# Kernel tuning notes

Hardware: AMD Instinct MI355X
Metric: run time of the kernel (lower is better)

The kernel has to match this reference:

```python
import jax, jax.numpy as jnp
import numpy as np

N_NODES = 100000
N_EDGES = 3200000


def gcn_conv(x, edge_index, W, b, n):
    # PyG GCNConv: h = x @ W; add self-loops; symmetric deg normalization; scatter-add; + bias
    src = edge_index[0]
    dst = edge_index[1]
    loop = jnp.arange(n, dtype=src.dtype)
    src = jnp.concatenate([src, loop])
    dst = jnp.concatenate([dst, loop])
    ones = jnp.ones(src.shape[0], dtype=x.dtype)
    deg = jax.ops.segment_sum(ones, dst, num_segments=n)  # in-degree with self-loops
    dinv = jnp.where(deg > 0, jax.lax.rsqrt(deg), 0.0)
    norm = dinv[src] * dinv[dst]  # [E+N]
    h = x @ W  # [N, out]
    msg = h[src] * norm[:, None]
    out = jax.ops.segment_sum(msg, dst, num_segments=n)
    return out + b


def setup_inputs() -> dict:
    key = jax.random.key(0)
    ks = jax.random.split(key, 8)
    x = jax.random.normal(ks[0], (N_NODES, 1024), dtype=jnp.float32)
    edge_index = jax.random.randint(ks[1], (2, N_EDGES), 0, N_NODES, dtype=jnp.int32)
    def glorot(k, fan_in, fan_out):
        s = jnp.sqrt(6.0 / (fan_in + fan_out))
        return jax.random.uniform(k, (fan_in, fan_out), jnp.float32, -s, s)
    W1 = glorot(ks[2], 1024, 128)
    W2 = glorot(ks[3], 128, 128)
    W3 = glorot(ks[4], 128, 9)
    b1 = jnp.zeros((128,), jnp.float32)
    b2 = jnp.zeros((128,), jnp.float32)
    b3 = jnp.zeros((9,), jnp.float32)
    return {"x": x, "edge_index": edge_index, "W1": W1, "b1": b1, "W2": W2, "b2": b2, "W3": W3, "b3": b3}


def reference(x, edge_index, W1, b1, W2, b2, W3, b3):
    n = x.shape[0]
    h = jax.nn.relu(gcn_conv(x, edge_index, W1, b1, n))
    h = jax.nn.relu(gcn_conv(h, edge_index, W2, b2, n))
    h = gcn_conv(h, edge_index, W3, b3, n)
    return jax.nn.log_softmax(h, axis=1)
```

## Files before the change

### kernel.cpp

```cpp
#include <hip/hip_runtime.h>
#include <hip/hip_bf16.h>

typedef __attribute__((ext_vector_type(8))) short bf16x8;
typedef __attribute__((ext_vector_type(4))) float f32x4;

#define BSH 8
#define BNODES 256

__device__ __forceinline__ unsigned short f2bf(float f) {
    union { float f; unsigned int u; } x; x.f = f;
    unsigned int u = x.u;
    unsigned int r = (u + 0x7fffu + ((u >> 16) & 1u)) >> 16;
    return (unsigned short)r;
}
__device__ __forceinline__ float bf_lo(unsigned int v) { return __uint_as_float(v << 16); }
__device__ __forceinline__ float bf_hi(unsigned int v) { return __uint_as_float(v & 0xffff0000u); }

__device__ __forceinline__ void gll16(const void* g, void* l) {
    __builtin_amdgcn_global_load_lds(
        (const __attribute__((address_space(1))) unsigned int*)g,
        (__attribute__((address_space(3))) unsigned int*)l, 16, 0, 0);
}


__global__ void k_zero(int* p, int n) {
    int i = blockIdx.x * 256 + threadIdx.x;
    if (i < n) p[i] = 0;
}

__global__ __launch_bounds__(256) void kA_hist(const int* __restrict__ dst, int* bhist,
                                               int E, int nbkt) {
    __shared__ int h[512];
    for (int i = threadIdx.x; i < 512; i += 256) h[i] = 0;
    __syncthreads();
    int stride = gridDim.x * 256;
    int n4 = E >> 2;
    for (int i = blockIdx.x * 256 + threadIdx.x; i < n4; i += stride) {
        int4 d = ((const int4*)dst)[i];
        atomicAdd(&h[d.x >> BSH], 1);
        atomicAdd(&h[d.y >> BSH], 1);
        atomicAdd(&h[d.z >> BSH], 1);
        atomicAdd(&h[d.w >> BSH], 1);
    }
    for (int i = (n4 << 2) + blockIdx.x * 256 + threadIdx.x; i < E; i += stride)
        atomicAdd(&h[dst[i] >> BSH], 1);
    __syncthreads();
    for (int i = threadIdx.x; i < nbkt; i += 256)
        if (h[i]) atomicAdd(&bhist[i], h[i]);
}

__global__ void kA_scan(const int* bhist, int* bbase, int* bcur, int nbkt) {
    __shared__ int s[512];
    int t = threadIdx.x;
    int v = (t < nbkt) ? bhist[t] : 0;
    s[t] = v;
    __syncthreads();
    for (int o = 1; o < 512; o <<= 1) {
        int x = (t >= o) ? s[t - o] : 0;
        __syncthreads();
        s[t] += x;
        __syncthreads();
    }
    if (t < nbkt) { bbase[t] = s[t] - v; bcur[t] = s[t] - v; }
    if (t == nbkt - 1) bbase[nbkt] = s[t];
}

#define TPE 16
__global__ __launch_bounds__(256) void kA_scatter(const int* __restrict__ src,
                                                  const int* __restrict__ dst,
                                                  int* bcur, unsigned int* pairs,
                                                  int E, int nbkt) {
    __shared__ int hist[512];
    __shared__ int base[512];
    const int tid = threadIdx.x;
    const int t0 = blockIdx.x * (256 * TPE);
    for (int i = tid; i < 512; i += 256) hist[i] = 0;
    __syncthreads();

    int es[TPE], ed[TPE], rk[TPE];
    bool valid[TPE];
    if (t0 + 256 * TPE <= E) {
        const int4* s4 = (const int4*)(src + t0 + tid * TPE);
        const int4* d4 = (const int4*)(dst + t0 + tid * TPE);
#pragma unroll
        for (int j = 0; j < TPE / 4; j++) {
            int4 a = s4[j], b = d4[j];
            es[4 * j + 0] = a.x; es[4 * j + 1] = a.y; es[4 * j + 2] = a.z; es[4 * j + 3] = a.w;
            ed[4 * j + 0] = b.x; ed[4 * j + 1] = b.y; ed[4 * j + 2] = b.z; ed[4 * j + 3] = b.w;
            valid[4 * j + 0] = valid[4 * j + 1] = valid[4 * j + 2] = valid[4 * j + 3] = true;
        }
    } else {
#pragma unroll
        for (int j = 0; j < TPE; j++) {
            int e = t0 + tid * TPE + j;
            valid[j] = (e < E);
            es[j] = valid[j] ? src[e] : 0;
            ed[j] = valid[j] ? dst[e] : 0;
        }
    }
#pragma unroll
    for (int j = 0; j < TPE; j++)
        if (valid[j]) rk[j] = atomicAdd(&hist[ed[j] >> BSH], 1);
    __syncthreads();
    for (int i = tid; i < nbkt; i += 256) {
        int c = hist[i];
        base[i] = c ? atomicAdd(&bcur[i], c) : 0;
    }
    __syncthreads();
#pragma unroll
    for (int j = 0; j < TPE; j++) {
        if (valid[j]) {
            int b = ed[j] >> BSH;
            unsigned int p = ((unsigned int)(ed[j] & (BNODES - 1)) << 24) | (unsigned int)es[j];
            pairs[base[b] + rk[j]] = p;
        }
    }
}

__global__ __launch_bounds__(512) void kB_group(const unsigned int* __restrict__ pairs,
                                                const int* __restrict__ bbase,
                                                int* csr, int* offs, int* cnt, float* dinv,
                                                int N, int nbkt) {
    int b = blockIdx.x;
    int p0 = bbase[b], p1 = bbase[b + 1];
    int node0 = b << BSH;
    int nn = min(BNODES, N - node0);
    __shared__ int lcnt[BNODES];
    __shared__ int ss[BNODES];
    __shared__ int lcur[BNODES];
    int t = threadIdx.x;
    if (t < BNODES) lcnt[t] = 0;
    __syncthreads();
    for (int i = p0 + t; i < p1; i += 512)
        atomicAdd(&lcnt[pairs[i] >> 24], 1);
    __syncthreads();
    int v = (t < BNODES) ? lcnt[t] : 0;
    if (t < BNODES) ss[t] = v;
    __syncthreads();
    for (int o = 1; o < BNODES; o <<= 1) {
        int x = (t >= o && t < BNODES) ? ss[t - o] : 0;
        __syncthreads();
        if (t < BNODES) ss[t] += x;
        __syncthreads();
    }
    if (t < nn) {
        int o = p0 + ss[t] - v;
        offs[node0 + t] = o;
        cnt[node0 + t] = v;
        dinv[node0 + t] = rsqrtf((float)(v + 1));
        lcur[t] = o;
    }
    __syncthreads();
    for (int i = p0 + t; i < p1; i += 512) {
        unsigned int p = pairs[i];
        int pos = atomicAdd(&lcur[p >> 24], 1);
        csr[pos] = (int)(p & 0xFFFFFFu);
    }
}

__global__ void k_wt(const float* W, unsigned short* Wt, int K, int C) {
    int i = blockIdx.x * 256 + threadIdx.x;
    if (i < K * C) {
        int k = i / C, c = i % C;
        Wt[(size_t)c * K + k] = f2bf(W[i]);
    }
}


template <int K, bool IN_F32>
__global__ __launch_bounds__(256) void k_gemm(const void* Xv, const unsigned short* Wt,
                                              const float* dinv, unsigned short* G, int M) {
    constexpr int ABYTES = IN_F32 ? 128 * 32 * 4 : 128 * 32 * 2;
    constexpr int BBYTES = 128 * 32 * 2;
    constexpr int NT = K / 32;
    __shared__ char smem[2 * ABYTES + 2 * BBYTES];

    const int tid = threadIdx.x;
    const int m0 = blockIdx.x * 128;
    const int w = tid >> 6, l = tid & 63, r = l & 15, kg = l >> 4;
    const int wb0 = tid & ~63;

    auto stage = [&](int buf, int k0) {
        if (IN_F32) {
            const float* X = (const float*)Xv;
            char* ab = smem + buf * ABYTES;
#pragma unroll
            for (int i = 0; i < 4; i++) {
                int wb = i * 256 + wb0;
                int c = wb + l;
                int row = c >> 3, slot = c & 7;
                int srow = m0 + row; if (srow >= M) srow = M - 1;
                gll16(X + (size_t)srow * K + k0 + slot * 4, ab + (size_t)wb * 16);
            }
        } else {
            const unsigned short* X = (const unsigned short*)Xv;
            char* ab = smem + buf * ABYTES;
#pragma unroll
            for (int i = 0; i < 2; i++) {
                int wb = i * 256 + wb0;
                int c = wb + l;
                int row = c >> 2, slot = c & 3;
                int srow = m0 + row; if (srow >= M) srow = M - 1;
                gll16(X + (size_t)srow * K + k0 + slot * 8, ab + (size_t)wb * 16);
            }
        }
        {
            char* bb = smem + 2 * ABYTES + buf * BBYTES;
#pragma unroll
            for (int i = 0; i < 2; i++) {
                int wb = i * 256 + wb0;
                int c = wb + l;
                int row = c >> 2, slot = c & 3;
                gll16(Wt + (size_t)row * K + k0 + slot * 8, bb + (size_t)wb * 16);
            }
        }
    };

    f32x4 acc[2][8];
#pragma unroll
    for (int mt = 0; mt < 2; mt++)
#pragma unroll
        for (int ct = 0; ct < 8; ct++) acc[mt][ct] = (f32x4){0.f, 0.f, 0.f, 0.f};

    stage(0, 0);
    __syncthreads();

    int cur = 0;
    for (int t = 0; t < NT; t++) {
        if (t + 1 < NT) stage(cur ^ 1, (t + 1) * 32);

        bf16x8 af[2], bfr[8];
        if (IN_F32) {
            const float* ab = (const float*)(smem + cur * ABYTES);
#pragma unroll
            for (int mt = 0; mt < 2; mt++) {
                int row = w * 32 + mt * 16 + r;
                float4 f0 = *(const float4*)(ab + row * 32 + kg * 8);
                float4 f1 = *(const float4*)(ab + row * 32 + kg * 8 + 4);
                union { bf16x8 v; unsigned short u[8]; } a;
                a.u[0] = f2bf(f0.x); a.u[1] = f2bf(f0.y); a.u[2] = f2bf(f0.z); a.u[3] = f2bf(f0.w);
                a.u[4] = f2bf(f1.x); a.u[5] = f2bf(f1.y); a.u[6] = f2bf(f1.z); a.u[7] = f2bf(f1.w);
                af[mt] = a.v;
            }
        } else {
            const unsigned short* ab = (const unsigned short*)(smem + cur * ABYTES);
#pragma unroll
            for (int mt = 0; mt < 2; mt++) {
                int row = w * 32 + mt * 16 + r;
                af[mt] = *(const bf16x8*)(ab + row * 32 + kg * 8);
            }
        }
        {
            const unsigned short* bb = (const unsigned short*)(smem + 2 * ABYTES + cur * BBYTES);
#pragma unroll
            for (int ct = 0; ct < 8; ct++)
                bfr[ct] = *(const bf16x8*)(bb + (ct * 16 + r) * 32 + kg * 8);
        }
#pragma unroll
        for (int mt = 0; mt < 2; mt++)
#pragma unroll
            for (int ct = 0; ct < 8; ct++)
                acc[mt][ct] = __builtin_amdgcn_mfma_f32_16x16x32_bf16(af[mt], bfr[ct], acc[mt][ct], 0, 0, 0);

        __syncthreads();
        cur ^= 1;
    }

#pragma unroll
    for (int mt = 0; mt < 2; mt++) {
        int rbase = m0 + w * 32 + mt * 16 + kg * 4;
        float dv[4];
#pragma unroll
        for (int q = 0; q < 4; q++) dv[q] = (rbase + q < M) ? dinv[rbase + q] : 0.f;
#pragma unroll
        for (int ct = 0; ct < 8; ct++) {
#pragma unroll
            for (int q = 0; q < 4; q++) {
                int gr = rbase + q;
                if (gr < M) G[(size_t)gr * 128 + ct * 16 + r] = f2bf(acc[mt][ct][q] * dv[q]);
            }
        }
    }
}


__global__ __launch_bounds__(256) void k_gemm3(const unsigned short* X3, const float* W3,
                                               const float* dinv, unsigned short* G3, int M) {
    __shared__ unsigned short sx[128 * 136];
    __shared__ float sw[128 * 9];
    int tid = threadIdx.x;
    int m0 = blockIdx.x * 128;
#pragma unroll
    for (int p = 0; p < 8; p++) {
        int idx = p * 256 + tid;
        int row = idx >> 4, c8 = idx & 15;
        uint4 v = make_uint4(0u, 0u, 0u, 0u);
        if (m0 + row < M) v = *(const uint4*)(X3 + (size_t)(m0 + row) * 128 + c8 * 8);
        *(uint4*)&sx[row * 136 + c8 * 8] = v;
    }
    for (int i = tid; i < 128 * 9; i += 256) sw[i] = W3[i];
    __syncthreads();

    int r = tid >> 1, h = tid & 1;
    float acc[9];
#pragma unroll
    for (int c = 0; c < 9; c++) acc[c] = 0.f;
    for (int kk = 0; kk < 64; kk++) {
        int k = h * 64 + kk;
        float xv = __uint_as_float(((unsigned int)sx[r * 136 + k]) << 16);
#pragma unroll
        for (int c = 0; c < 9; c++) acc[c] += xv * sw[k * 9 + c];
    }
#pragma unroll
    for (int c = 0; c < 9; c++) acc[c] += __shfl_xor(acc[c], 1);
    int gr = m0 + r;
    if (h == 0 && gr < M) {
        float dv = dinv[gr];
#pragma unroll
        for (int c = 0; c < 9; c++) G3[(size_t)gr * 16 + c] = f2bf(acc[c] * dv);
#pragma unroll
        for (int c = 9; c < 16; c++) G3[(size_t)gr * 16 + c] = 0;
    }
}


#define A128_CAP 1024

__global__ __launch_bounds__(256) void k_agg128(const unsigned int* __restrict__ gv,
                                                const int* __restrict__ csr,
                                                const int* __restrict__ offs,
                                                const int* __restrict__ cnt,
                                                const float* __restrict__ dinv,
                                                const float* __restrict__ bias,
                                                unsigned int* xout, int N, int do_relu) {
    __shared__ int sidx[A128_CAP];
    const int tid = threadIdx.x;
    const int n0 = blockIdx.x * 4;
    const int nlast = min(n0 + 3, N - 1);
    const int base = offs[n0];
    const int tot = offs[nlast] + cnt[nlast] - base;
    const bool lds_ok = (tot <= A128_CAP);
    if (lds_ok)
        for (int i = tid; i < tot; i += 256) sidx[i] = csr[base + i];
    __syncthreads();

    const int node = n0 + (tid >> 6);
    if (node >= N) return;
    const int l = tid & 63;
    const int ne = cnt[node];
    const int st = offs[node] - base;

    unsigned int u = gv[node * 64 + l];
    float a0 = bf_lo(u), a1 = bf_hi(u);
    int e = 0;
    if (lds_ok) {
        for (; e + 8 <= ne; e += 8) {
            int s0 = sidx[st + e], s1 = sidx[st + e + 1];
            int s2 = sidx[st + e + 2], s3 = sidx[st + e + 3];
            int s4 = sidx[st + e + 4], s5 = sidx[st + e + 5];
            int s6 = sidx[st + e + 6], s7 = sidx[st + e + 7];
            unsigned int v0 = gv[s0 * 64 + l], v1 = gv[s1 * 64 + l];
            unsigned int v2 = gv[s2 * 64 + l], v3 = gv[s3 * 64 + l];
            unsigned int v4 = gv[s4 * 64 + l], v5 = gv[s5 * 64 + l];
            unsigned int v6 = gv[s6 * 64 + l], v7 = gv[s7 * 64 + l];
            a0 += bf_lo(v0); a1 += bf_hi(v0);
            a0 += bf_lo(v1); a1 += bf_hi(v1);
            a0 += bf_lo(v2); a1 += bf_hi(v2);
            a0 += bf_lo(v3); a1 += bf_hi(v3);
            a0 += bf_lo(v4); a1 += bf_hi(v4);
            a0 += bf_lo(v5); a1 += bf_hi(v5);
            a0 += bf_lo(v6); a1 += bf_hi(v6);
            a0 += bf_lo(v7); a1 += bf_hi(v7);
        }
        for (; e < ne; e++) {
            unsigned int v = gv[sidx[st + e] * 64 + l];
            a0 += bf_lo(v); a1 += bf_hi(v);
        }
    } else {
        const int gst = offs[node];
        for (; e < ne; e++) {
            unsigned int v = gv[csr[gst + e] * 64 + l];
            a0 += bf_lo(v); a1 += bf_hi(v);
        }
    }
    float dv = dinv[node];
    float o0 = fmaf(dv, a0, bias[2 * l]);
    float o1 = fmaf(dv, a1, bias[2 * l + 1]);
    if (do_relu) { o0 = fmaxf(o0, 0.f); o1 = fmaxf(o1, 0.f); }
    xout[node * 64 + l] = (unsigned int)f2bf(o0) | ((unsigned int)f2bf(o1) << 16);
}


#define A9_CAP 3072

__global__ __launch_bounds__(256) void k_agg9(const unsigned int* __restrict__ g3v,
                                              const int* __restrict__ csr,
                                              const int* __restrict__ offs,
                                              const int* __restrict__ cnt,
                                              const float* __restrict__ dinv,
                                              const float* __restrict__ b3,
                                              float* out, int N) {
    __shared__ int sidx[A9_CAP];
    const int tid = threadIdx.x;
    const int n0 = blockIdx.x * 32;
    const int nlast = min(n0 + 31, N - 1);
    const int base = offs[n0];
    const int tot = offs[nlast] + cnt[nlast] - base;
    const bool lds_ok = (tot <= A9_CAP);
    if (lds_ok)
        for (int i = tid; i < tot; i += 256) sidx[i] = csr[base + i];
    __syncthreads();

    const int node = n0 + (tid >> 3);
    if (node >= N) return;
    const int jl = tid & 7;
    const int ne = cnt[node];

    unsigned int u = g3v[node * 8 + jl];
    float a0 = bf_lo(u), a1 = bf_hi(u);
    int e = 0;
    if (lds_ok) {
        const int st = offs[node] - base;
        for (; e + 4 <= ne; e += 4) {
            int s0 = sidx[st + e], s1 = sidx[st + e + 1];
            int s2 = sidx[st + e + 2], s3 = sidx[st + e + 3];
            unsigned int v0 = g3v[s0 * 8 + jl], v1 = g3v[s1 * 8 + jl];
            unsigned int v2 = g3v[s2 * 8 + jl], v3 = g3v[s3 * 8 + jl];
            a0 += bf_lo(v0); a1 += bf_hi(v0);
            a0 += bf_lo(v1); a1 += bf_hi(v1);
            a0 += bf_lo(v2); a1 += bf_hi(v2);
            a0 += bf_lo(v3); a1 += bf_hi(v3);
        }
        for (; e < ne; e++) {
            unsigned int v = g3v[sidx[st + e] * 8 + jl];
            a0 += bf_lo(v); a1 += bf_hi(v);
        }
    } else {
        const int gst = offs[node];
        for (; e < ne; e++) {
            unsigned int v = g3v[csr[gst + e] * 8 + jl];
            a0 += bf_lo(v); a1 += bf_hi(v);
        }
    }
    float dv = dinv[node];
    int c0 = 2 * jl, c1 = 2 * jl + 1;
    float o0 = (c0 < 9) ? fmaf(dv, a0, b3[c0]) : -INFINITY;
    float o1 = (c1 < 9) ? fmaf(dv, a1, b3[c1]) : -INFINITY;
    float m = fmaxf(o0, o1);
    for (int d = 1; d < 8; d <<= 1) m = fmaxf(m, __shfl_xor(m, d));
    float s = 0.f;
    if (c0 < 9) s += expf(o0 - m);
    if (c1 < 9) s += expf(o1 - m);
    for (int d = 1; d < 8; d <<= 1) s += __shfl_xor(s, d);
    float ls = m + logf(s);
    if (c0 < 9) out[(size_t)node * 9 + c0] = o0 - ls;
    if (c1 < 9) out[(size_t)node * 9 + c1] = o1 - ls;
}


extern "C" void kernel_launch(void* const* d_in, const int* in_sizes, int n_in,
                              void* d_out, int out_size, void* d_ws, size_t ws_size,
                              hipStream_t stream) {
    const float* x = (const float*)d_in[0];
    const int* ei = (const int*)d_in[1];
    const float* W1 = (const float*)d_in[2];
    const float* b1 = (const float*)d_in[3];
    const float* W2 = (const float*)d_in[4];
    const float* b2 = (const float*)d_in[5];
    const float* W3 = (const float*)d_in[6];
    const float* b3 = (const float*)d_in[7];
    float* out = (float*)d_out;

    const int N = in_sizes[0] / 1024;
    const int E = in_sizes[1] / 2;
    const int* src = ei;
    const int* dst = ei + E;
    const int nbkt = (N + BNODES - 1) >> BSH;

    char* ws = (char*)d_ws;
    size_t off = 0;
    auto alloc = [&](size_t bytes) -> char* {
        char* p = ws + off;
        off += (bytes + 255) & ~(size_t)255;
        return p;
    };
    int* cnt = (int*)alloc((size_t)N * 4);
    int* offs = (int*)alloc((size_t)N * 4);
    float* dinv = (float*)alloc((size_t)N * 4);
    int* bhist = (int*)alloc(520 * 4);
    int* bbase = (int*)alloc(520 * 4);
    int* bcur = (int*)alloc(520 * 4);
    unsigned int* pairs = (unsigned int*)alloc((size_t)E * 4);
    int* csr = (int*)alloc((size_t)E * 4);
    unsigned short* w1t = (unsigned short*)alloc(128 * 1024 * 2);
    unsigned short* w2t = (unsigned short*)alloc(128 * 128 * 2);
    unsigned short* gbuf = (unsigned short*)alloc((size_t)N * 128 * 2);
    unsigned short* xbuf = (unsigned short*)alloc((size_t)N * 128 * 2);
    unsigned short* g3 = (unsigned short*)alloc((size_t)N * 16 * 2);

    const int MB = (N + 127) / 128;
    const int AB = (N + 3) / 4;
    const int AB9 = (N + 31) / 32;
    const int SB = (E + 256 * TPE - 1) / (256 * TPE);

    k_zero<<<3, 256, 0, stream>>>(bhist, 520);
    kA_hist<<<512, 256, 0, stream>>>(dst, bhist, E, nbkt);
    kA_scan<<<1, 512, 0, stream>>>(bhist, bbase, bcur, nbkt);
    kA_scatter<<<SB, 256, 0, stream>>>(src, dst, bcur, pairs, E, nbkt);
    kB_group<<<nbkt, 512, 0, stream>>>(pairs, bbase, csr, offs, cnt, dinv, N, nbkt);
    k_wt<<<(1024 * 128 + 255) / 256, 256, 0, stream>>>(W1, w1t, 1024, 128);
    k_wt<<<(128 * 128 + 255) / 256, 256, 0, stream>>>(W2, w2t, 128, 128);

    k_gemm<1024, true><<<MB, 256, 0, stream>>>((const void*)x, w1t, dinv, gbuf, N);
    k_agg128<<<AB, 256, 0, stream>>>((const unsigned int*)gbuf, csr, offs, cnt, dinv, b1,
                                     (unsigned int*)xbuf, N, 1);
    k_gemm<128, false><<<MB, 256, 0, stream>>>((const void*)xbuf, w2t, dinv, gbuf, N);
    k_agg128<<<AB, 256, 0, stream>>>((const unsigned int*)gbuf, csr, offs, cnt, dinv, b2,
                                     (unsigned int*)xbuf, N, 1);
    k_gemm3<<<MB, 256, 0, stream>>>(xbuf, W3, dinv, g3, N);
    k_agg9<<<AB9, 256, 0, stream>>>((const unsigned int*)g3, csr, offs, cnt, dinv, b3, out, N);
}
```

Measured before the change: 503.0 us.

## Load GEMM operands directly from global into registers, dropping LDS staging

Replaces the double-buffered global_load_lds staging in the GEMM kernel with per-lane direct global loads of the A rows and the W fragments into registers, removing LDS traffic and block barriers. It also merges the two weight-transpose launches into one kernel. In exchange each wave now reads W fragments from global/L2 on its own, with no reuse through LDS, and the fp32 A loads are strided per lane, which may hurt coalescing and memory-level parallelism.

```diff
diff --git a/kernel.cpp b/kernel.cpp
--- a/kernel.cpp
+++ b/kernel.cpp
@@ -15,12 +15,6 @@
 }
 __device__ __forceinline__ float bf_lo(unsigned int v) { return __uint_as_float(v << 16); }
 __device__ __forceinline__ float bf_hi(unsigned int v) { return __uint_as_float(v & 0xffff0000u); }
-
-__device__ __forceinline__ void gll16(const void* g, void* l) {
-    __builtin_amdgcn_global_load_lds(
-        (const __attribute__((address_space(1))) unsigned int*)g,
-        (__attribute__((address_space(3))) unsigned int*)l, 16, 0, 0);
-}
 
 
 __global__ void k_zero(int* p, int n) {
@@ -158,11 +152,18 @@
     }
 }
 
-__global__ void k_wt(const float* W, unsigned short* Wt, int K, int C) {
+__global__ void k_wt2(const float* __restrict__ W1, unsigned short* w1t,
+                      const float* __restrict__ W2, unsigned short* w2t) {
     int i = blockIdx.x * 256 + threadIdx.x;
-    if (i < K * C) {
-        int k = i / C, c = i % C;
-        Wt[(size_t)c * K + k] = f2bf(W[i]);
+    if (i < 1024 * 128) {
+        int k = i >> 7, c = i & 127;
+        w1t[c * 1024 + k] = f2bf(W1[i]);
+    } else {
+        int j = i - 1024 * 128;
+        if (j < 128 * 128) {
+            int k = j >> 7, c = j & 127;
+            w2t[c * 128 + k] = f2bf(W2[j]);
+        }
     }
 }
 
@@ -170,51 +171,14 @@
 template <int K, bool IN_F32>
 __global__ __launch_bounds__(256) void k_gemm(const void* Xv, const unsigned short* Wt,
                                               const float* dinv, unsigned short* G, int M) {
-    constexpr int ABYTES = IN_F32 ? 128 * 32 * 4 : 128 * 32 * 2;
-    constexpr int BBYTES = 128 * 32 * 2;
-    constexpr int NT = K / 32;
-    __shared__ char smem[2 * ABYTES + 2 * BBYTES];
-
     const int tid = threadIdx.x;
     const int m0 = blockIdx.x * 128;
     const int w = tid >> 6, l = tid & 63, r = l & 15, kg = l >> 4;
-    const int wb0 = tid & ~63;
-
-    auto stage = [&](int buf, int k0) {
-        if (IN_F32) {
-            const float* X = (const float*)Xv;
-            char* ab = smem + buf * ABYTES;
-#pragma unroll
-            for (int i = 0; i < 4; i++) {
-                int wb = i * 256 + wb0;
-                int c = wb + l;
-                int row = c >> 3, slot = c & 7;
-                int srow = m0 + row; if (srow >= M) srow = M - 1;
-                gll16(X + (size_t)srow * K + k0 + slot * 4, ab + (size_t)wb * 16);
-            }
-        } else {
-            const unsigned short* X = (const unsigned short*)Xv;
-            char* ab = smem + buf * ABYTES;
-#pragma unroll
-            for (int i = 0; i < 2; i++) {
-                int wb = i * 256 + wb0;
-                int c = wb + l;
-                int row = c >> 2, slot = c & 3;
-                int srow = m0 + row; if (srow >= M) srow = M - 1;
-                gll16(X + (size_t)srow * K + k0 + slot * 8, ab + (size_t)wb * 16);
-            }
-        }
-        {
-            char* bb = smem + 2 * ABYTES + buf * BBYTES;
-#pragma unroll
-            for (int i = 0; i < 2; i++) {
-                int wb = i * 256 + wb0;
-                int c = wb + l;
-                int row = c >> 2, slot = c & 3;
-                gll16(Wt + (size_t)row * K + k0 + slot * 8, bb + (size_t)wb * 16);
-            }
-        }
-    };
+
+    const int row0 = m0 + w * 32 + r;
+    const int row1 = row0 + 16;
+    const int cr0 = min(row0, M - 1);
+    const int cr1 = min(row1, M - 1);
 
     f32x4 acc[2][8];
 #pragma unroll
@@ -222,48 +186,53 @@
 #pragma unroll
         for (int ct = 0; ct < 8; ct++) acc[mt][ct] = (f32x4){0.f, 0.f, 0.f, 0.f};
 
-    stage(0, 0);
-    __syncthreads();
-
-    int cur = 0;
-    for (int t = 0; t < NT; t++) {
-        if (t + 1 < NT) stage(cur ^ 1, (t + 1) * 32);
-
-        bf16x8 af[2], bfr[8];
-        if (IN_F32) {
-            const float* ab = (const float*)(smem + cur * ABYTES);
-#pragma unroll
-            for (int mt = 0; mt < 2; mt++) {
-                int row = w * 32 + mt * 16 + r;
-                float4 f0 = *(const float4*)(ab + row * 32 + kg * 8);
-                float4 f1 = *(const float4*)(ab + row * 32 + kg * 8 + 4);
-                union { bf16x8 v; unsigned short u[8]; } a;
-                a.u[0] = f2bf(f0.x); a.u[1] = f2bf(f0.y); a.u[2] = f2bf(f0.z); a.u[3] = f2bf(f0.w);
-                a.u[4] = f2bf(f1.x); a.u[5] = f2bf(f1.y); a.u[6] = f2bf(f1.z); a.u[7] = f2bf(f1.w);
-                af[mt] = a.v;
-            }
-        } else {
-            const unsigned short* ab = (const unsigned short*)(smem + cur * ABYTES);
-#pragma unroll
-            for (int mt = 0; mt < 2; mt++) {
-                int row = w * 32 + mt * 16 + r;
-                af[mt] = *(const bf16x8*)(ab + row * 32 + kg * 8);
-            }
-        }
-        {
-            const unsigned short* bb = (const unsigned short*)(smem + 2 * ABYTES + cur * BBYTES);
-#pragma unroll
-            for (int ct = 0; ct < 8; ct++)
-                bfr[ct] = *(const bf16x8*)(bb + (ct * 16 + r) * 32 + kg * 8);
-        }
-#pragma unroll
-        for (int mt = 0; mt < 2; mt++)
-#pragma unroll
-            for (int ct = 0; ct < 8; ct++)
-                acc[mt][ct] = __builtin_amdgcn_mfma_f32_16x16x32_bf16(af[mt], bfr[ct], acc[mt][ct], 0, 0, 0);
-
-        __syncthreads();
-        cur ^= 1;
+    const unsigned short* bp = Wt + (size_t)r * K + kg * 8;
+
+    if (IN_F32) {
+        const float* X = (const float*)Xv;
+        const float* a0 = X + (size_t)cr0 * K + kg * 8;
+        const float* a1 = X + (size_t)cr1 * K + kg * 8;
+#pragma unroll 2
+        for (int k0 = 0; k0 < K; k0 += 32) {
+            float4 f00 = *(const float4*)(a0 + k0);
+            float4 f01 = *(const float4*)(a0 + k0 + 4);
+            float4 f10 = *(const float4*)(a1 + k0);
+            float4 f11 = *(const float4*)(a1 + k0 + 4);
+            bf16x8 bfr[8];
+#pragma unroll
+            for (int ct = 0; ct < 8; ct++)
+                bfr[ct] = *(const bf16x8*)(bp + (size_t)ct * 16 * K + k0);
+            union { bf16x8 v; unsigned short u[8]; } A0, A1;
+            A0.u[0] = f2bf(f00.x); A0.u[1] = f2bf(f00.y); A0.u[2] = f2bf(f00.z); A0.u[3] = f2bf(f00.w);
+            A0.u[4] = f2bf(f01.x); A0.u[5] = f2bf(f01.y); A0.u[6] = f2bf(f01.z); A0.u[7] = f2bf(f01.w);
+            A1.u[0] = f2bf(f10.x); A1.u[1] = f2bf(f10.y); A1.u[2] = f2bf(f10.z); A1.u[3] = f2bf(f10.w);
+            A1.u[4] = f2bf(f11.x); A1.u[5] = f2bf(f11.y); A1.u[6] = f2bf(f11.z); A1.u[7] = f2bf(f11.w);
+#pragma unroll
+            for (int ct = 0; ct < 8; ct++)
+                acc[0][ct] = __builtin_amdgcn_mfma_f32_16x16x32_bf16(A0.v, bfr[ct], acc[0][ct], 0, 0, 0);
+#pragma unroll
+            for (int ct = 0; ct < 8; ct++)
+                acc[1][ct] = __builtin_amdgcn_mfma_f32_16x16x32_bf16(A1.v, bfr[ct], acc[1][ct], 0, 0, 0);
+        }
+    } else {
+        const unsigned short* X = (const unsigned short*)Xv;
+        const unsigned short* a0 = X + (size_t)cr0 * K + kg * 8;
+        const unsigned short* a1 = X + (size_t)cr1 * K + kg * 8;
+#pragma unroll 2
+        for (int k0 = 0; k0 < K; k0 += 32) {
+            bf16x8 af0 = *(const bf16x8*)(a0 + k0);
+            bf16x8 af1 = *(const bf16x8*)(a1 + k0);
+            bf16x8 bfr[8];
+#pragma unroll
+            for (int ct = 0; ct < 8; ct++)
+                bfr[ct] = *(const bf16x8*)(bp + (size_t)ct * 16 * K + k0);
+#pragma unroll
+            for (int ct = 0; ct < 8; ct++)
+                acc[0][ct] = __builtin_amdgcn_mfma_f32_16x16x32_bf16(af0, bfr[ct], acc[0][ct], 0, 0, 0);
+#pragma unroll
+            for (int ct = 0; ct < 8; ct++)
+                acc[1][ct] = __builtin_amdgcn_mfma_f32_16x16x32_bf16(af1, bfr[ct], acc[1][ct], 0, 0, 0);
+        }
     }
 
 #pragma unroll
@@ -502,14 +471,14 @@
     const int AB = (N + 3) / 4;
     const int AB9 = (N + 31) / 32;
     const int SB = (E + 256 * TPE - 1) / (256 * TPE);
+    const int WB = (1024 * 128 + 128 * 128 + 255) / 256;
 
     k_zero<<<3, 256, 0, stream>>>(bhist, 520);
     kA_hist<<<512, 256, 0, stream>>>(dst, bhist, E, nbkt);
     kA_scan<<<1, 512, 0, stream>>>(bhist, bbase, bcur, nbkt);
     kA_scatter<<<SB, 256, 0, stream>>>(src, dst, bcur, pairs, E, nbkt);
     kB_group<<<nbkt, 512, 0, stream>>>(pairs, bbase, csr, offs, cnt, dinv, N, nbkt);
-    k_wt<<<(1024 * 128 + 255) / 256, 256, 0, stream>>>(W1, w1t, 1024, 128);
-    k_wt<<<(128 * 128 + 255) / 256, 256, 0, stream>>>(W2, w2t, 128, 128);
+    k_wt2<<<WB, 256, 0, stream>>>(W1, w1t, W2, w2t);
 
     k_gemm<1024, true><<<MB, 256, 0, stream>>>((const void*)x, w1t, dinv, gbuf, N);
     k_agg128<<<AB, 256, 0, stream>>>((const unsigned int*)gbuf, csr, offs, cnt, dinv, b1,
```

New measurement: 591.1 us. 17.5% more time.

## Deepen GEMM prefetch to four LDS buffers with vmcnt waits; fuse weight transposes

Applied to the files above, without the earlier changes.

The bf16 MFMA GEMM moves from a double-buffered loop with a full __syncthreads per tile to a four-buffer ring. Three tiles are prefetched ahead with global_load_lds, and each step waits on an explicit s_waitcnt vmcnt count plus a bare s_barrier. The goal is to keep more global loads in flight, mainly in the layer-1 GEMM that streams the large fp32 input. The trade-off is that LDS per block doubles, which can lower occupancy, and correctness now depends on the hand-counted vmcnt values. The two weight-transpose launches are also merged into one kernel to save a launch.

```diff
diff --git a/kernel.cpp b/kernel.cpp
--- a/kernel.cpp
+++ b/kernel.cpp
@@ -20,6 +20,15 @@
     __builtin_amdgcn_global_load_lds(
         (const __attribute__((address_space(1))) unsigned int*)g,
         (__attribute__((address_space(3))) unsigned int*)l, 16, 0, 0);
+}
+
+template <int N> __device__ __forceinline__ void waitvm() {
+    if constexpr (N == 0) asm volatile("s_waitcnt vmcnt(0)" ::: "memory");
+    else if constexpr (N == 4) asm volatile("s_waitcnt vmcnt(4)" ::: "memory");
+    else if constexpr (N == 6) asm volatile("s_waitcnt vmcnt(6)" ::: "memory");
+    else if constexpr (N == 8) asm volatile("s_waitcnt vmcnt(8)" ::: "memory");
+    else if constexpr (N == 12) asm volatile("s_waitcnt vmcnt(12)" ::: "memory");
+    else static_assert(N == 0, "unhandled vmcnt");
 }
 
 
@@ -158,22 +167,34 @@
     }
 }
 
-__global__ void k_wt(const float* W, unsigned short* Wt, int K, int C) {
+__global__ void k_wt2(const float* __restrict__ W1, unsigned short* w1t,
+                      const float* __restrict__ W2, unsigned short* w2t) {
     int i = blockIdx.x * 256 + threadIdx.x;
-    if (i < K * C) {
-        int k = i / C, c = i % C;
-        Wt[(size_t)c * K + k] = f2bf(W[i]);
+    if (i < 1024 * 128) {
+        int k = i >> 7, c = i & 127;
+        w1t[c * 1024 + k] = f2bf(W1[i]);
+    } else {
+        int j = i - 1024 * 128;
+        if (j < 128 * 128) {
+            int k = j >> 7, c = j & 127;
+            w2t[c * 128 + k] = f2bf(W2[j]);
+        }
     }
 }
 
 
 template <int K, bool IN_F32>
-__global__ __launch_bounds__(256) void k_gemm(const void* Xv, const unsigned short* Wt,
-                                              const float* dinv, unsigned short* G, int M) {
+__global__ __launch_bounds__(256) void k_gemm(const void* __restrict__ Xv,
+                                              const unsigned short* __restrict__ Wt,
+                                              const float* __restrict__ dinv,
+                                              unsigned short* __restrict__ G, int M) {
     constexpr int ABYTES = IN_F32 ? 128 * 32 * 4 : 128 * 32 * 2;
     constexpr int BBYTES = 128 * 32 * 2;
     constexpr int NT = K / 32;
-    __shared__ char smem[2 * ABYTES + 2 * BBYTES];
+    constexpr int NBUF = 4;
+    constexpr int L = IN_F32 ? 6 : 4;
+    static_assert(NT >= 3, "pipeline needs >=3 tiles");
+    __shared__ char smem[NBUF * (ABYTES + BBYTES)];
 
     const int tid = threadIdx.x;
     const int m0 = blockIdx.x * 128;
@@ -205,7 +226,7 @@
             }
         }
         {
-            char* bb = smem + 2 * ABYTES + buf * BBYTES;
+            char* bb = smem + NBUF * ABYTES + buf * BBYTES;
 #pragma unroll
             for (int i = 0; i < 2; i++) {
                 int wb = i * 256 + wb0;
@@ -222,16 +243,10 @@
 #pragma unroll
         for (int ct = 0; ct < 8; ct++) acc[mt][ct] = (f32x4){0.f, 0.f, 0.f, 0.f};
 
-    stage(0, 0);
-    __syncthreads();
-
-    int cur = 0;
-    for (int t = 0; t < NT; t++) {
-        if (t + 1 < NT) stage(cur ^ 1, (t + 1) * 32);
-
+    auto compute = [&](int buf) {
         bf16x8 af[2], bfr[8];
         if (IN_F32) {
-            const float* ab = (const float*)(smem + cur * ABYTES);
+            const float* ab = (const float*)(smem + buf * ABYTES);
 #pragma unroll
             for (int mt = 0; mt < 2; mt++) {
                 int row = w * 32 + mt * 16 + r;
@@ -243,7 +258,7 @@
                 af[mt] = a.v;
             }
         } else {
-            const unsigned short* ab = (const unsigned short*)(smem + cur * ABYTES);
+            const unsigned short* ab = (const unsigned short*)(smem + buf * ABYTES);
 #pragma unroll
             for (int mt = 0; mt < 2; mt++) {
                 int row = w * 32 + mt * 16 + r;
@@ -251,7 +266,7 @@
             }
         }
         {
-            const unsigned short* bb = (const unsigned short*)(smem + 2 * ABYTES + cur * BBYTES);
+            const unsigned short* bb = (const unsigned short*)(smem + NBUF * ABYTES + buf * BBYTES);
 #pragma unroll
             for (int ct = 0; ct < 8; ct++)
                 bfr[ct] = *(const bf16x8*)(bb + (ct * 16 + r) * 32 + kg * 8);
@@ -261,10 +276,28 @@
 #pragma unroll
             for (int ct = 0; ct < 8; ct++)
                 acc[mt][ct] = __builtin_amdgcn_mfma_f32_16x16x32_bf16(af[mt], bfr[ct], acc[mt][ct], 0, 0, 0);
-
-        __syncthreads();
-        cur ^= 1;
-    }
+    };
+
+    stage(0, 0);
+    stage(1, 32);
+    stage(2, 64);
+
+    int t = 0;
+    for (; t + 3 < NT; ++t) {
+        waitvm<2 * L>();
+        __builtin_amdgcn_s_barrier();
+        compute(t & 3);
+        stage((t + 3) & 3, (t + 3) * 32);
+    }
+    waitvm<2 * L>();
+    __builtin_amdgcn_s_barrier();
+    compute((NT - 3) & 3);
+    waitvm<L>();
+    __builtin_amdgcn_s_barrier();
+    compute((NT - 2) & 3);
+    waitvm<0>();
+    __builtin_amdgcn_s_barrier();
+    compute((NT - 1) & 3);
 
 #pragma unroll
     for (int mt = 0; mt < 2; mt++) {
@@ -502,14 +535,14 @@
     const int AB = (N + 3) / 4;
     const int AB9 = (N + 31) / 32;
     const int SB = (E + 256 * TPE - 1) / (256 * TPE);
+    const int WB = (1024 * 128 + 128 * 128 + 255) / 256;
 
     k_zero<<<3, 256, 0, stream>>>(bhist, 520);
     kA_hist<<<512, 256, 0, stream>>>(dst, bhist, E, nbkt);
     kA_scan<<<1, 512, 0, stream>>>(bhist, bbase, bcur, nbkt);
     kA_scatter<<<SB, 256, 0, stream>>>(src, dst, bcur, pairs, E, nbkt);
     kB_group<<<nbkt, 512, 0, stream>>>(pairs, bbase, csr, offs, cnt, dinv, N, nbkt);
-    k_wt<<<(1024 * 128 + 255) / 256, 256, 0, stream>>>(W1, w1t, 1024, 128);
-    k_wt<<<(128 * 128 + 255) / 256, 256, 0, stream>>>(W2, w2t, 128, 128);
+    k_wt2<<<WB, 256, 0, stream>>>(W1, w1t, W2, w2t);
 
     k_gemm<1024, true><<<MB, 256, 0, stream>>>((const void*)x, w1t, dinv, gbuf, N);
     k_agg128<<<AB, 256, 0, stream>>>((const unsigned int*)gbuf, csr, offs, cnt, dinv, b1,
```

Result: slower. 526.5 us (+4.7%).
